# Performance work log

Hardware: AMD Instinct MI355X
Metric: run time of the kernel (lower is better)

## Reference

```python
import jax, jax.numpy as jnp
import numpy as np


def setup_inputs() -> dict:
    key = jax.random.key(0)
    k1, k2 = jax.random.split(key)
    x = jax.random.normal(k1, (32, 3, 512, 512), dtype=jnp.float32)
    p = jax.random.uniform(k2, (32, 4), dtype=jnp.float32)
    return {"x": x, "p": p}


def _reflect(coord, size):
    # PyTorch grid_sample reflection padding, align_corners=False:
    # reflect about borders at -0.5 and size-0.5 (span = size), then clip.
    span = float(size)
    c = jnp.abs(coord + 0.5)
    flips = jnp.floor(c / span)
    extra = c - flips * span
    c = jnp.where(jnp.mod(flips, 2.0) == 0.0, extra, span - extra) - 0.5
    return jnp.clip(c, 0.0, size - 1.0)


def _bilinear_sample(img, ix, iy, W, H):
    # img: [C,H,W]; ix,iy: [H,W] pixel-space coords already reflected into [0,size-1]
    ix0f = jnp.floor(ix)
    iy0f = jnp.floor(iy)
    fx = ix - ix0f
    fy = iy - iy0f
    x0 = jnp.clip(ix0f.astype(jnp.int32), 0, W - 1)
    x1 = jnp.clip(ix0f.astype(jnp.int32) + 1, 0, W - 1)
    y0 = jnp.clip(iy0f.astype(jnp.int32), 0, H - 1)
    y1 = jnp.clip(iy0f.astype(jnp.int32) + 1, 0, H - 1)
    v00 = img[:, y0, x0]  # [C,H,W]
    v01 = img[:, y0, x1]
    v10 = img[:, y1, x0]
    v11 = img[:, y1, x1]
    return (v00 * (1.0 - fx) * (1.0 - fy)
            + v01 * fx * (1.0 - fy)
            + v10 * (1.0 - fx) * fy
            + v11 * fx * fy)


def reference(x, p):
    B, C, H, W = x.shape
    tx, ty, th, ts = p[:, 0], p[:, 1], p[:, 2], p[:, 3]
    c, s = jnp.cos(th), jnp.sin(th)
    # affine_grid base coords, align_corners=False: centers of pixels in [-1,1]
    xs = (jnp.arange(W, dtype=x.dtype) + 0.5) * (2.0 / W) - 1.0  # [W]
    ys = (jnp.arange(H, dtype=x.dtype) + 0.5) * (2.0 / H) - 1.0  # [H]
    a = (ts * c)[:, None, None]
    b = (-ts * s)[:, None, None]
    d = (ts * s)[:, None, None]
    e = (ts * c)[:, None, None]
    gx = a * xs[None, None, :] + b * ys[None, :, None] + tx[:, None, None]  # [B,H,W]
    gy = d * xs[None, None, :] + e * ys[None, :, None] + ty[:, None, None]  # [B,H,W]
    # unnormalize to pixel space (align_corners=False)
    ix = ((gx + 1.0) * W - 1.0) * 0.5
    iy = ((gy + 1.0) * H - 1.0) * 0.5
    ix = _reflect(ix, W)
    iy = _reflect(iy, H)
    out = jax.vmap(lambda img, jx, jy: _bilinear_sample(img, jx, jy, W, H))(x, ix, iy)
    return out
```

## Files before the change

### kernel.cpp

```cpp
#include <hip/hip_runtime.h>


#define B_ 32
#define C_ 3
#define H_ 512
#define W_ 512
#define TILE 32
#define LSTRIDE 60
#define MAXROWS 55
#define BUFW (MAXROWS * LSTRIDE + 64)

typedef float f32x4 __attribute__((ext_vector_type(4)));

__device__ __forceinline__ float reflect512(float coord) {
    const float c = fabsf(coord + 0.5f);
    const float m = c - floorf(c * (1.0f / 1024.0f)) * 1024.0f;
    const float t = 512.0f - fabsf(m - 512.0f);
    return fminf(fmaxf(t - 0.5f, 0.0f), 511.0f);
}

__global__ __launch_bounds__(256, 5)
void st_kernel(const float* __restrict__ x, const float* __restrict__ p,
               float* __restrict__ out) {
    __shared__ float smem[2 * BUFW];

    const int tid = threadIdx.x;

    const int bid = blockIdx.x;
    const int wid = (bid & 7) * 1024 + (bid >> 3);
    const int b   = wid >> 8;
    const int til = wid & 255;
    const int tlx = til & 15;
    const int tly = til >> 4;

    const float tx = p[b * 4 + 0];
    const float ty = p[b * 4 + 1];
    const float th = p[b * 4 + 2];
    const float ts = p[b * 4 + 3];
    const float cth = __cosf(th), sth = __sinf(th);
    const float a  =  ts * cth;
    const float bb = -ts * sth;
    const float d  =  ts * sth;

    const float xs_c = ((float)(tlx * TILE) + 16.0f) * (2.0f / W_) - 1.0f;
    const float ys_c = ((float)(tly * TILE) + 16.0f) * (2.0f / H_) - 1.0f;
    const float gxc = a * xs_c + bb * ys_c + tx;
    const float gyc = d * xs_c + a  * ys_c + ty;
    const float rcx = reflect512(((gxc + 1.0f) * W_ - 1.0f) * 0.5f);
    const float rcy = reflect512(((gyc + 1.0f) * H_ - 1.0f) * 0.5f);
    const float ext = 16.0f * (fabsf(a) + fabsf(bb)) + 3.0f;

    int bx0 = max((int)floorf(rcx - ext), 0) & ~3;
    const int xhi = min((int)ceilf(rcx + ext) + 1, W_);
    int nw4 = (xhi - bx0 + 3) >> 2;
    nw4 = min(min(nw4, 15), (W_ - bx0) >> 2);

    int by0 = max((int)floorf(rcy - ext), 0);
    const int yhi = min((int)ceilf(rcy + ext) + 1, H_);
    const int nrows = min(yhi - by0, MAXROWS);

    const size_t plane = (size_t)H_ * W_;
    const float* img = x + (size_t)b * C_ * plane;
    const size_t gbase = (size_t)by0 * W_ + bx0;
    const int c4 = tid & 15;
    const int r0 = tid >> 4;

    {
        const float* gp = img + gbase;
        for (int r = r0; r < nrows; r += 16)
            if (c4 < nw4)
                *reinterpret_cast<f32x4*>(&smem[r * LSTRIDE + c4 * 4]) =
                    *reinterpret_cast<const f32x4*>(gp + (size_t)r * W_ + c4 * 4);
        if (nw4 < 15)
            for (int r = r0; r < nrows; r += 16)
                if (c4 == nw4) {
                    *reinterpret_cast<f32x4*>(&smem[r * LSTRIDE + c4 * 4]) = (f32x4)(0.0f);
                    *reinterpret_cast<f32x4*>(&smem[BUFW + r * LSTRIDE + c4 * 4]) = (f32x4)(0.0f);
                }
        if (tid < 16) {
            *reinterpret_cast<f32x4*>(&smem[nrows * LSTRIDE + tid * 4]) = (f32x4)(0.0f);
            *reinterpret_cast<f32x4*>(&smem[BUFW + nrows * LSTRIDE + tid * 4]) = (f32x4)(0.0f);
        }
    }

    const int lr   = tid >> 3;
    const int lc   = (tid & 7) * 4;
    const int row  = tly * TILE + lr;
    const int col0 = tlx * TILE + lc;

    const float ysn = ((float)row  + 0.5f) * (2.0f / H_) - 1.0f;
    const float xsn = ((float)col0 + 0.5f) * (2.0f / W_) - 1.0f;
    float ix = ((a * xsn + bb * ysn + tx + 1.0f) * W_ - 1.0f) * 0.5f;
    float iy = ((d * xsn + a  * ysn + ty + 1.0f) * H_ - 1.0f) * 0.5f;

    const int koff = by0 * LSTRIDE + bx0;
    int   idx4[4];
    float w00_[4], w01_[4], w10_[4], w11_[4];
    #pragma unroll
    for (int k = 0; k < 4; ++k) {
        const float rx  = reflect512(ix);
        const float ry  = reflect512(iy);
        const float x0f = floorf(rx);
        const float y0f = floorf(ry);
        const float fx  = rx - x0f;
        const float fy  = ry - y0f;
        const float ox  = 1.0f - fx;
        const float oy  = 1.0f - fy;
        w00_[k] = ox * oy; w01_[k] = fx * oy; w10_[k] = ox * fy; w11_[k] = fx * fy;
        idx4[k] = (int)y0f * LSTRIDE + (int)x0f - koff;
        ix += a;
        iy += d;
    }

    float* outp = out + (size_t)b * C_ * plane + (size_t)row * W_ + col0;

    f32x4 vr[4];
    auto load_regs = [&](int ch) {
        const float* gp = img + (size_t)ch * plane + gbase;
        #pragma unroll
        for (int i = 0; i < 4; ++i) {
            const int rr = min(r0 + i * 16, nrows - 1);
            vr[i] = (c4 < nw4)
                ? *reinterpret_cast<const f32x4*>(gp + (size_t)rr * W_ + c4 * 4)
                : (f32x4)(0.0f);
        }
    };
    auto write_regs = [&](float* base) {
        #pragma unroll
        for (int i = 0; i < 4; ++i) {
            const int r = r0 + i * 16;
            if (r < nrows && c4 < nw4)
                *reinterpret_cast<f32x4*>(base + r * LSTRIDE + c4 * 4) = vr[i];
        }
    };
    auto compute_store = [&](int ch, const float* base) {
        float acc[4];
        #pragma unroll
        for (int k = 0; k < 4; ++k) {
            const float* s = base + idx4[k];
            acc[k] = s[0] * w00_[k] + s[1] * w01_[k]
                   + s[LSTRIDE] * w10_[k] + s[LSTRIDE + 1] * w11_[k];
        }
        const f32x4 v = {acc[0], acc[1], acc[2], acc[3]};
        __builtin_nontemporal_store(v, reinterpret_cast<f32x4*>(outp + (size_t)ch * plane));
    };

    __syncthreads();

    load_regs(1);
    compute_store(0, smem);
    write_regs(smem + BUFW);
    __syncthreads();

    load_regs(2);
    compute_store(1, smem + BUFW);
    write_regs(smem);
    __syncthreads();

    compute_store(2, smem);
}

extern "C" void kernel_launch(void* const* d_in, const int* in_sizes, int n_in,
                              void* d_out, int out_size, void* d_ws, size_t ws_size,
                              hipStream_t stream) {
    const float* x = (const float*)d_in[0];
    const float* p = (const float*)d_in[1];
    float* out = (float*)d_out;

    dim3 block(256, 1, 1);
    dim3 grid((W_ / TILE) * (H_ / TILE) * B_, 1, 1);
    st_kernel<<<grid, block, 0, stream>>>(x, p, out);
}
```

Baseline: 186.7 us.

## Single-buffer shared memory and raise occupancy target with per-channel reload

Replaces the double-buffered shared tile with a single buffer, halving LDS use, and raises the launch-bounds block target from 5 to 8 per CU. The first channel's loads are issued into registers before the coordinate math so they overlap it. Bilinear weights are recomputed per channel from stored fractions to cut register pressure, loads use clamped column indices, and stores become regular instead of nontemporal. The trade-off is an extra barrier per channel, since the next channel can only be written after all threads finish reading the current one, so less latency is hidden within a block.

```diff
diff --git a/kernel.cpp b/kernel.cpp
--- a/kernel.cpp
+++ b/kernel.cpp
@@ -8,7 +8,7 @@
 #define TILE 32
 #define LSTRIDE 60
 #define MAXROWS 55
-#define BUFW (MAXROWS * LSTRIDE + 64)
+#define SMEMW (MAXROWS * LSTRIDE + 64)
 
 typedef float f32x4 __attribute__((ext_vector_type(4)));
 
@@ -19,10 +19,10 @@
     return fminf(fmaxf(t - 0.5f, 0.0f), 511.0f);
 }
 
-__global__ __launch_bounds__(256, 5)
+__global__ __launch_bounds__(256, 8)
 void st_kernel(const float* __restrict__ x, const float* __restrict__ p,
                float* __restrict__ out) {
-    __shared__ float smem[2 * BUFW];
+    __shared__ float smem[SMEMW];
 
     const int tid = threadIdx.x;
 
@@ -61,26 +61,16 @@
 
     const size_t plane = (size_t)H_ * W_;
     const float* img = x + (size_t)b * C_ * plane;
-    const size_t gbase = (size_t)by0 * W_ + bx0;
     const int c4 = tid & 15;
     const int r0 = tid >> 4;
+    const int ccl = min(c4, max(nw4 - 1, 0)) * 4;
+    const float* gp0 = img + (size_t)by0 * W_ + bx0;
 
-    {
-        const float* gp = img + gbase;
-        for (int r = r0; r < nrows; r += 16)
-            if (c4 < nw4)
-                *reinterpret_cast<f32x4*>(&smem[r * LSTRIDE + c4 * 4]) =
-                    *reinterpret_cast<const f32x4*>(gp + (size_t)r * W_ + c4 * 4);
-        if (nw4 < 15)
-            for (int r = r0; r < nrows; r += 16)
-                if (c4 == nw4) {
-                    *reinterpret_cast<f32x4*>(&smem[r * LSTRIDE + c4 * 4]) = (f32x4)(0.0f);
-                    *reinterpret_cast<f32x4*>(&smem[BUFW + r * LSTRIDE + c4 * 4]) = (f32x4)(0.0f);
-                }
-        if (tid < 16) {
-            *reinterpret_cast<f32x4*>(&smem[nrows * LSTRIDE + tid * 4]) = (f32x4)(0.0f);
-            *reinterpret_cast<f32x4*>(&smem[BUFW + nrows * LSTRIDE + tid * 4]) = (f32x4)(0.0f);
-        }
+    f32x4 vr[4];
+    #pragma unroll
+    for (int i = 0; i < 4; ++i) {
+        const int rr = min(r0 + i * 16, nrows - 1);
+        vr[i] = *reinterpret_cast<const f32x4*>(gp0 + (size_t)rr * W_ + ccl);
     }
 
     const int lr   = tid >> 3;
@@ -95,69 +85,72 @@
 
     const int koff = by0 * LSTRIDE + bx0;
     int   idx4[4];
-    float w00_[4], w01_[4], w10_[4], w11_[4];
+    float fx_[4], fy_[4];
     #pragma unroll
     for (int k = 0; k < 4; ++k) {
         const float rx  = reflect512(ix);
         const float ry  = reflect512(iy);
         const float x0f = floorf(rx);
         const float y0f = floorf(ry);
-        const float fx  = rx - x0f;
-        const float fy  = ry - y0f;
-        const float ox  = 1.0f - fx;
-        const float oy  = 1.0f - fy;
-        w00_[k] = ox * oy; w01_[k] = fx * oy; w10_[k] = ox * fy; w11_[k] = fx * fy;
+        fx_[k] = rx - x0f;
+        fy_[k] = ry - y0f;
         idx4[k] = (int)y0f * LSTRIDE + (int)x0f - koff;
         ix += a;
         iy += d;
     }
 
-    float* outp = out + (size_t)b * C_ * plane + (size_t)row * W_ + col0;
-
-    f32x4 vr[4];
-    auto load_regs = [&](int ch) {
-        const float* gp = img + (size_t)ch * plane + gbase;
-        #pragma unroll
-        for (int i = 0; i < 4; ++i) {
-            const int rr = min(r0 + i * 16, nrows - 1);
-            vr[i] = (c4 < nw4)
-                ? *reinterpret_cast<const f32x4*>(gp + (size_t)rr * W_ + c4 * 4)
-                : (f32x4)(0.0f);
-        }
-    };
-    auto write_regs = [&](float* base) {
+    #pragma unroll
+    for (int i = 0; i < 4; ++i) {
+        const int r = r0 + i * 16;
+        if (r < nrows && c4 < nw4)
+            *reinterpret_cast<f32x4*>(&smem[r * LSTRIDE + c4 * 4]) = vr[i];
+    }
+    if (nw4 < 15) {
         #pragma unroll
         for (int i = 0; i < 4; ++i) {
             const int r = r0 + i * 16;
-            if (r < nrows && c4 < nw4)
-                *reinterpret_cast<f32x4*>(base + r * LSTRIDE + c4 * 4) = vr[i];
+            if (r < nrows && c4 == nw4)
+                *reinterpret_cast<f32x4*>(&smem[r * LSTRIDE + c4 * 4]) = (f32x4)(0.0f);
         }
-    };
-    auto compute_store = [&](int ch, const float* base) {
+    }
+    if (tid < 16)
+        *reinterpret_cast<f32x4*>(&smem[nrows * LSTRIDE + tid * 4]) = (f32x4)(0.0f);
+
+    float* outp = out + (size_t)b * C_ * plane + (size_t)row * W_ + col0;
+
+    #pragma unroll
+    for (int ch = 0; ch < C_; ++ch) {
+        __syncthreads();
+
         float acc[4];
         #pragma unroll
         for (int k = 0; k < 4; ++k) {
-            const float* s = base + idx4[k];
-            acc[k] = s[0] * w00_[k] + s[1] * w01_[k]
-                   + s[LSTRIDE] * w10_[k] + s[LSTRIDE + 1] * w11_[k];
+            const float fx = fx_[k], fy = fy_[k];
+            const float ox = 1.0f - fx, oy = 1.0f - fy;
+            const float* s = &smem[idx4[k]];
+            acc[k] = s[0] * (ox * oy) + s[1] * (fx * oy)
+                   + s[LSTRIDE] * (ox * fy) + s[LSTRIDE + 1] * (fx * fy);
         }
         const f32x4 v = {acc[0], acc[1], acc[2], acc[3]};
-        __builtin_nontemporal_store(v, reinterpret_cast<f32x4*>(outp + (size_t)ch * plane));
-    };
+        *reinterpret_cast<f32x4*>(outp + (size_t)ch * plane) = v;
 
-    __syncthreads();
-
-    load_regs(1);
-    compute_store(0, smem);
-    write_regs(smem + BUFW);
-    __syncthreads();
-
-    load_regs(2);
-    compute_store(1, smem + BUFW);
-    write_regs(smem);
-    __syncthreads();
-
-    compute_store(2, smem);
+        if (ch < C_ - 1) {
+            const float* gp = img + (size_t)(ch + 1) * plane
+                                  + (size_t)by0 * W_ + bx0;
+            #pragma unroll
+            for (int i = 0; i < 4; ++i) {
+                const int rr = min(r0 + i * 16, nrows - 1);
+                vr[i] = *reinterpret_cast<const f32x4*>(gp + (size_t)rr * W_ + ccl);
+            }
+            __syncthreads();
+            #pragma unroll
+            for (int i = 0; i < 4; ++i) {
+                const int r = r0 + i * 16;
+                if (r < nrows && c4 < nw4)
+                    *reinterpret_cast<f32x4*>(&smem[r * LSTRIDE + c4 * 4]) = vr[i];
+            }
+        }
+    }
 }
 
 extern "C" void kernel_launch(void* const* d_in, const int* in_sizes, int n_in,
```

After: 179.7 us. -3.7%, faster.
